# Performance work log

Hardware: AMD Instinct MI355X
Metric: run time of the kernel (lower is better)

The kernel has to match this reference:

```python
import jax, jax.numpy as jnp
import numpy as np
from jax import lax

WINDOW_SIZE = 11
SIGMA = 1.5
LEVELS = 5
WEIGHTS = jnp.array([0.0448, 0.2856, 0.3001, 0.2363, 0.1333], dtype=jnp.float32)


def _make_window(ws, channel):
    # 1D gaussian, sigma=1.5, normalized; outer product -> 2D window, tiled per channel
    x = jnp.arange(ws, dtype=jnp.float32) - ws // 2
    g = jnp.exp(-(x * x) / (2.0 * SIGMA * SIGMA))
    g = g / g.sum()
    w2 = jnp.outer(g, g)  # [ws, ws]
    return jnp.broadcast_to(w2[None, None], (channel, 1, ws, ws))


def _dwconv(x, win, channel):
    # depthwise VALID conv, matches F.conv2d(..., padding=0, groups=channel)
    return lax.conv_general_dilated(
        x, win, window_strides=(1, 1), padding='VALID',
        feature_group_count=channel,
        dimension_numbers=('NCHW', 'OIHW', 'NCHW'))


def _ssim_cs(img1, img2):
    # dynamic data range, as in the torch source (L=1 for [0,1) inputs)
    max_val = jnp.where(jnp.max(img1) > 128.0, 255.0, 1.0)
    min_val = jnp.where(jnp.min(img1) < -0.5, -1.0, 0.0)
    L = max_val - min_val

    n, c, h, w = img1.shape
    ws = min(WINDOW_SIZE, h, w)  # static python int
    win = _make_window(ws, c)

    mu1 = _dwconv(img1, win, c)
    mu2 = _dwconv(img2, win, c)
    mu1_sq = mu1 * mu1
    mu2_sq = mu2 * mu2
    mu1_mu2 = mu1 * mu2
    sigma1_sq = _dwconv(img1 * img1, win, c) - mu1_sq
    sigma2_sq = _dwconv(img2 * img2, win, c) - mu2_sq
    sigma12 = _dwconv(img1 * img2, win, c) - mu1_mu2

    C1 = (0.01 * L) ** 2
    C2 = (0.03 * L) ** 2
    v1 = 2.0 * sigma12 + C2
    v2 = sigma1_sq + sigma2_sq + C2
    cs = jnp.mean(v1 / v2)
    ssim_map = (2.0 * mu1_mu2 + C1) * v1 / ((mu1_sq + mu2_sq + C1) * v2)
    return jnp.mean(ssim_map), cs


def _avg_pool2(x):
    # F.avg_pool2d(x, (2,2)): stride 2, no padding (floors odd dims)
    n, c, h, w = x.shape
    x = x[:, :, : (h // 2) * 2, : (w // 2) * 2]
    return x.reshape(n, c, h // 2, 2, w // 2, 2).mean(axis=(3, 5))


def setup_inputs() -> dict:
    key = jax.random.key(0)
    k1, k2 = jax.random.split(key)
    img1 = jax.random.uniform(k1, (16, 3, 512, 512), dtype=jnp.float32)
    img2 = jax.random.uniform(k2, (16, 3, 512, 512), dtype=jnp.float32)
    return {"img1": img1, "img2": img2}


def reference(img1, img2):
    mssim, mcs = [], []
    for _ in range(LEVELS):  # fixed 5-level pyramid, shapes shrink each level
        s, c = _ssim_cs(img1, img2)
        mssim.append(s)
        mcs.append(c)
        img1 = _avg_pool2(img1)
        img2 = _avg_pool2(img2)
    mssim = (jnp.stack(mssim) + 1.0) / 2.0  # normalize=True
    mcs = (jnp.stack(mcs) + 1.0) / 2.0
    pow1 = mcs ** WEIGHTS
    pow2 = mssim ** WEIGHTS
    # NOTE: faithful to source: prod over (pow1[:-1] * pow2[-1]) broadcasts pow2[-1]
    return jnp.prod(pow1[:-1] * pow2[-1])
```

## Files before the change

### kernel.cpp

```cpp
#include <hip/hip_runtime.h>


#define NTHR 512

typedef float v4  __attribute__((ext_vector_type(4)));
typedef float v2f __attribute__((ext_vector_type(2)));

__device__ __forceinline__ float frcp(float x) { return __builtin_amdgcn_rcpf(x); }

#define GW_DEF const float GW[11] = {0.00102840f, 0.00759877f, 0.03600070f, \
    0.10936069f, 0.21300636f, 0.26601172f, 0.21300636f, 0.10936069f,        \
    0.03600070f, 0.00759877f, 0.00102840f};

__device__ __forceinline__ void conv11(const float* s, const float* d,
                                       v4& hs, v4& hd, v4& hss, v4& hdd)
{
    GW_DEF
    #pragma unroll
    for (int j = 0; j < 11; ++j) {
        float w = GW[j];
        v4 sv = {s[j], s[j+1], s[j+2], s[j+3]};
        v4 dv = {d[j], d[j+1], d[j+2], d[j+3]};
        v4 wsv = w * sv, wdv = w * dv;
        hs += wsv; hd += wdv; hss += wsv * sv; hdd += wdv * dv;
    }
}

template<int TROWS>
__device__ void hpass_direct(const float* __restrict__ p1, const float* __restrict__ p2,
                             int H, int tx0, int ty0, v4* hb)
{
    constexpr int HR = TROWS + 10;
    for (int task = threadIdx.x; task < HR * 8; task += NTHR) {
        const int r = task >> 3, cg2 = task & 7;
        const int gr = ty0 + r;
        const int c0 = tx0 + cg2 * 4;
        v4 hs = 0.f, hd = 0.f, hss = 0.f, hdd = 0.f;
        if (gr < H) {
            float s[16], d[16];
            if (c0 + 16 <= H) {
                const float* pa = p1 + (size_t)gr * H + c0;
                const float* pb = p2 + (size_t)gr * H + c0;
                #pragma unroll
                for (int q = 0; q < 4; ++q) {
                    v4 va = *(const v4*)(pa + 4 * q);
                    v4 vb = *(const v4*)(pb + 4 * q);
                    v4 sv = va + vb, dv = va - vb;
                    s[4*q+0] = sv.x; s[4*q+1] = sv.y; s[4*q+2] = sv.z; s[4*q+3] = sv.w;
                    d[4*q+0] = dv.x; d[4*q+1] = dv.y; d[4*q+2] = dv.z; d[4*q+3] = dv.w;
                }
            } else {
                #pragma unroll
                for (int q = 0; q < 16; ++q) {
                    int cc = c0 + q;
                    float a = (cc < H) ? p1[(size_t)gr * H + cc] : 0.f;
                    float b = (cc < H) ? p2[(size_t)gr * H + cc] : 0.f;
                    s[q] = a + b; d[q] = a - b;
                }
            }
            conv11(s, d, hs, hd, hss, hdd);
        }
        v4* row = &hb[r * 33 + cg2 * 4];
        row[0] = (v4){hs.x, hd.x, hss.x, hdd.x};
        row[1] = (v4){hs.y, hd.y, hss.y, hdd.y};
        row[2] = (v4){hs.z, hd.z, hss.z, hdd.z};
        row[3] = (v4){hs.w, hd.w, hss.w, hdd.w};
    }
}

template<int TROWS>
__device__ void hpass_pool1(const float* __restrict__ q1, const float* __restrict__ q2,
                            int H, int tx0, int ty0, v4* hb)
{
    constexpr int HR = TROWS + 10;
    const int HS = 2 * H;
    for (int task = threadIdx.x; task < HR * 8; task += NTHR) {
        const int r = task >> 3, cg2 = task & 7;
        const int gr = ty0 + r;
        const int c0 = tx0 + cg2 * 4;
        v4 hs = 0.f, hd = 0.f, hss = 0.f, hdd = 0.f;
        if (gr < H) {
            float s[16], d[16];
            const int iy = 2 * gr;
            if (c0 + 16 <= H) {
                const float* a0 = q1 + (size_t)iy * HS + 2 * c0;
                const float* b0 = q2 + (size_t)iy * HS + 2 * c0;
                #pragma unroll
                for (int q = 0; q < 8; ++q) {
                    v4 xa0 = *(const v4*)(a0 + 4 * q);
                    v4 xa1 = *(const v4*)(a0 + HS + 4 * q);
                    v4 xb0 = *(const v4*)(b0 + 4 * q);
                    v4 xb1 = *(const v4*)(b0 + HS + 4 * q);
                    float pa0 = 0.25f * ((xa0.x + xa0.y) + (xa1.x + xa1.y));
                    float pa1 = 0.25f * ((xa0.z + xa0.w) + (xa1.z + xa1.w));
                    float pb0 = 0.25f * ((xb0.x + xb0.y) + (xb1.x + xb1.y));
                    float pb1 = 0.25f * ((xb0.z + xb0.w) + (xb1.z + xb1.w));
                    s[2*q]   = pa0 + pb0; d[2*q]   = pa0 - pb0;
                    s[2*q+1] = pa1 + pb1; d[2*q+1] = pa1 - pb1;
                }
            } else {
                #pragma unroll
                for (int q = 0; q < 16; ++q) {
                    int cc = c0 + q;
                    float pa = 0.f, pb = 0.f;
                    if (cc < H) {
                        const float* qa = q1 + (size_t)iy * HS + 2 * cc;
                        const float* qb = q2 + (size_t)iy * HS + 2 * cc;
                        pa = 0.25f * ((qa[0] + qa[1]) + (qa[HS] + qa[HS + 1]));
                        pb = 0.25f * ((qb[0] + qb[1]) + (qb[HS] + qb[HS + 1]));
                    }
                    s[q] = pa + pb; d[q] = pa - pb;
                }
            }
            conv11(s, d, hs, hd, hss, hdd);
        }
        v4* row = &hb[r * 33 + cg2 * 4];
        row[0] = (v4){hs.x, hd.x, hss.x, hdd.x};
        row[1] = (v4){hs.y, hd.y, hss.y, hdd.y};
        row[2] = (v4){hs.z, hd.z, hss.z, hdd.z};
        row[3] = (v4){hs.w, hd.w, hss.w, hdd.w};
    }
}

template<int TROWS>
__device__ void hpass_lds(const float* la, const float* lb,
                          int H, int tx0, int ty0, v4* hb)
{
    constexpr int HR = TROWS + 10;
    for (int task = threadIdx.x; task < HR * 8; task += NTHR) {
        const int r = task >> 3, cg2 = task & 7;
        const int gr = ty0 + r;
        const int c0 = tx0 + cg2 * 4;
        v4 hs = 0.f, hd = 0.f, hss = 0.f, hdd = 0.f;
        if (gr < H) {
            float s[16], d[16];
            const int lr = 2 * r;
            #pragma unroll
            for (int q = 0; q < 16; ++q) {
                int cc = c0 + q;
                float pa = 0.f, pb = 0.f;
                if (cc < H) {
                    int lc = 2 * (cc - tx0);
                    const float* a0 = la + lr * 89 + lc;
                    const float* b0 = lb + lr * 89 + lc;
                    pa = 0.25f * ((a0[0] + a0[1]) + (a0[89] + a0[90]));
                    pb = 0.25f * ((b0[0] + b0[1]) + (b0[89] + b0[90]));
                }
                s[q] = pa + pb; d[q] = pa - pb;
            }
            conv11(s, d, hs, hd, hss, hdd);
        }
        v4* row = &hb[r * 33 + cg2 * 4];
        row[0] = (v4){hs.x, hd.x, hss.x, hdd.x};
        row[1] = (v4){hs.y, hd.y, hss.y, hdd.y};
        row[2] = (v4){hs.z, hd.z, hss.z, hdd.z};
        row[3] = (v4){hs.w, hd.w, hss.w, hdd.w};
    }
}

__device__ void stage_pool1(const float* __restrict__ s1, const float* __restrict__ s2,
                            int DL, int tx0, int ty0, float* la, float* lb)
{
    const int SD = 2 * DL;
    for (int t = threadIdx.x; t < 2 * 52 * 44; t += NTHR) {
        int im = t >= 52 * 44; int tt = im ? t - 52 * 44 : t;
        int rr = tt / 44, cp = tt % 44;
        int xr = 2 * ty0 + rr, xc = 2 * tx0 + 2 * cp;
        const float* sp = im ? s2 : s1;
        float* lp = im ? lb : la;
        float v0 = 0.f, v1 = 0.f;
        if (xr < DL && xc < DL) {
            const float* q0 = sp + (size_t)(2 * xr) * SD + 2 * xc;
            v4 r0 = *(const v4*)q0;
            v4 r1 = *(const v4*)(q0 + SD);
            v0 = 0.25f * ((r0.x + r0.y) + (r1.x + r1.y));
            v1 = 0.25f * ((r0.z + r0.w) + (r1.z + r1.w));
        }
        lp[rr * 89 + 2 * cp]     = v0;
        lp[rr * 89 + 2 * cp + 1] = v1;
    }
}

__device__ void stage_pool2(const float* __restrict__ s1, const float* __restrict__ s2,
                            int DL, int ty0, float* la, float* lb)
{
    const int SD = 4 * DL;
    for (int t = threadIdx.x; t < 2 * 52 * 88; t += NTHR) {
        int im = t >= 52 * 88; int tt = im ? t - 52 * 88 : t;
        int rr = tt / 88, cc = tt % 88;
        int yr = 2 * ty0 + rr, yc = cc;
        const float* sp = im ? s2 : s1;
        float* lp = im ? lb : la;
        float v = 0.f;
        if (yr < DL && yc < DL) {
            const float* q = sp + (size_t)(4 * yr) * SD + 4 * yc;
            v4 r0 = *(const v4*)q;
            v4 r1 = *(const v4*)(q + SD);
            v4 r2 = *(const v4*)(q + 2 * SD);
            v4 r3 = *(const v4*)(q + 3 * SD);
            float a00 = 0.25f * ((r0.x + r0.y) + (r1.x + r1.y));
            float a01 = 0.25f * ((r0.z + r0.w) + (r1.z + r1.w));
            float a10 = 0.25f * ((r2.x + r2.y) + (r3.x + r3.y));
            float a11 = 0.25f * ((r2.z + r2.w) + (r3.z + r3.w));
            v = 0.25f * ((a00 + a01) + (a10 + a11));
        }
        lp[rr * 89 + cc] = v;
    }
}

template<int TROWS>
__device__ void vpass_reduce(int H, int tx0, int ty0, const v4* hb, float* red,
                             float* __restrict__ partS, float* __restrict__ partC)
{
    constexpr int OPT = TROWS * 32 / NTHR;
    constexpr int NW  = NTHR / 64;
    GW_DEF
    const float C1 = 1e-4f, C2 = 9e-4f;
    const int tid   = threadIdx.x;
    const int outHW = H - 10;
    const int col   = tid & 31;
    const int row0  = (tid >> 5) * OPT;
    const float colm = (tx0 + col < outHW) ? 1.f : 0.f;
    v4 A[OPT];
    #pragma unroll
    for (int k = 0; k < OPT; ++k) A[k] = 0.f;

    #pragma unroll
    for (int r = 0; r < OPT + 10; ++r) {
        v4 h = hb[(row0 + r) * 33 + col];
        #pragma unroll
        for (int k = 0; k < OPT; ++k) {
            const int j = r - k;
            if (j >= 0 && j < 11) A[k] += GW[j] * h;
        }
    }

    float ssim_t = 0.f, cs_t = 0.f;
    #pragma unroll
    for (int k = 0; k < OPT; ++k) {
        float mask = colm * ((ty0 + row0 + k < outHW) ? 1.f : 0.f);
        float mu_s = A[k].x, mu_d = A[k].y;
        float P = mu_s * mu_s, Q = mu_d * mu_d;
        float U = A[k].z - P, V = A[k].w - Q;
        float v1 = 0.5f * (U - V) + C2;
        float v2 = 0.5f * (U + V) + C2;
        float n1 = 0.5f * (P - Q) + C1;
        float d1 = 0.5f * (P + Q) + C1;
        float csv = v1 * frcp(v2);
        float ssv = n1 * csv * frcp(d1);
        cs_t   += mask * csv;
        ssim_t += mask * ssv;
    }

    #pragma unroll
    for (int off = 32; off > 0; off >>= 1) {
        ssim_t += __shfl_down(ssim_t, off);
        cs_t   += __shfl_down(cs_t, off);
    }
    int wave = tid >> 6, lane = tid & 63;
    if (lane == 0) { red[wave] = ssim_t; red[NW + wave] = cs_t; }
    __syncthreads();
    if (tid == 0) {
        float s = 0.f, c = 0.f;
        #pragma unroll
        for (int w = 0; w < NW; ++w) { s += red[w]; c += red[NW + w]; }
        partS[0] = s; partC[0] = c;
    }
}

__global__ __launch_bounds__(NTHR, 8) void l0_kernel(
    const float* __restrict__ img1, const float* __restrict__ img2,
    float* __restrict__ x1a, float* __restrict__ x1b,
    float* __restrict__ accS, float* __restrict__ accC)
{
    __shared__ v4 hb[74 * 33];
    __shared__ float red[16];

    const int tid = threadIdx.x;
    const int nc  = blockIdx.z;
    const int tx0 = blockIdx.x * 32;
    const int ty0 = blockIdx.y * 64;
    const int H   = 512;
    const float* p1 = img1 + (size_t)nc * H * H;
    const float* p2 = img2 + (size_t)nc * H * H;

    {
        const int r = tid >> 4, c = tid & 15;
        const int iy = ty0 + 2 * r, ix = tx0 + 2 * c;
        v2f a0 = *(const v2f*)(p1 + (size_t)iy * H + ix);
        v2f a1 = *(const v2f*)(p1 + (size_t)(iy + 1) * H + ix);
        v2f b0 = *(const v2f*)(p2 + (size_t)iy * H + ix);
        v2f b1 = *(const v2f*)(p2 + (size_t)(iy + 1) * H + ix);
        size_t o = (size_t)nc * 256 * 256 + (size_t)((ty0 >> 1) + r) * 256 + ((tx0 >> 1) + c);
        x1a[o] = 0.25f * ((a0.x + a0.y) + (a1.x + a1.y));
        x1b[o] = 0.25f * ((b0.x + b0.y) + (b1.x + b1.y));
    }

    hpass_direct<64>(p1, p2, H, tx0, ty0, hb);
    __syncthreads();
    int fb = (int)blockIdx.x + 16 * ((int)blockIdx.y + 8 * nc);
    vpass_reduce<64>(H, tx0, ty0, hb, red, accS + fb, accC + fb);
}

__global__ __launch_bounds__(NTHR, 6) void tail_kernel(
    const float* __restrict__ x1a, const float* __restrict__ x1b,
    float* __restrict__ accTS, float* __restrict__ accTC)
{
    __shared__ v4 smemv[3172];
    __shared__ float red[16];
    v4* hb    = smemv;
    float* la = (float*)smemv + 3432;
    float* lb = la + 52 * 89;

    const int b = (int)blockIdx.x;
    if (b < 1536) {
        const int H = 256;
        int cx = b & 7, rem = b >> 3, cy = rem & 3, nc = rem >> 2;
        const float* p1 = x1a + (size_t)nc * H * H;
        const float* p2 = x1b + (size_t)nc * H * H;
        int tx0 = cx * 32, ty0 = cy * 64;
        hpass_direct<64>(p1, p2, H, tx0, ty0, hb);
        __syncthreads();
        vpass_reduce<64>(H, tx0, ty0, hb, red, accTS + b, accTC + b);
    } else if (b < 2304) {
        const int H = 128;
        int lbk = b - 1536;
        int cx = lbk & 3, rem = lbk >> 2, cy = rem & 3, nc = rem >> 2;
        const float* q1 = x1a + (size_t)nc * 256 * 256;
        const float* q2 = x1b + (size_t)nc * 256 * 256;
        int tx0 = cx * 32, ty0 = cy * 32;
        hpass_pool1<32>(q1, q2, H, tx0, ty0, hb);
        __syncthreads();
        vpass_reduce<32>(H, tx0, ty0, hb, red, accTS + b, accTC + b);
    } else if (b < 2688) {
        const int H = 64;
        int lbk = b - 2304;
        int cx = lbk & 1, rem = lbk >> 1, cy = rem & 3, nc = rem >> 2;
        const float* q1 = x1a + (size_t)nc * 256 * 256;
        const float* q2 = x1b + (size_t)nc * 256 * 256;
        int tx0 = cx * 32, ty0 = cy * 16;
        stage_pool1(q1, q2, 128, tx0, ty0, la, lb);
        __syncthreads();
        hpass_lds<16>(la, lb, H, tx0, ty0, hb);
        __syncthreads();
        vpass_reduce<16>(H, tx0, ty0, hb, red, accTS + b, accTC + b);
    } else {
        const int H = 32;
        int lbk = b - 2688;
        int cy = lbk & 1, nc = lbk >> 1;
        const float* q1 = x1a + (size_t)nc * 256 * 256;
        const float* q2 = x1b + (size_t)nc * 256 * 256;
        int tx0 = 0, ty0 = cy * 16;
        stage_pool2(q1, q2, 64, ty0, la, lb);
        __syncthreads();
        hpass_lds<16>(la, lb, H, tx0, ty0, hb);
        __syncthreads();
        vpass_reduce<16>(H, tx0, ty0, hb, red, accTS + b, accTC + b);
    }
}

__global__ void finalize_kernel(const float* __restrict__ acc0S, const float* __restrict__ acc0C,
                                const float* __restrict__ accTS, const float* __restrict__ accTC,
                                float* __restrict__ out)
{
    __shared__ float sm[10];
    __shared__ float wred[8];
    const int tid  = (int)threadIdx.x;
    const int wave = tid >> 6, lane = tid & 63;
    const int st[5] = {0, 0, 1536, 2304, 2688};
    const int en[5] = {6144, 1536, 2304, 2688, 2784};

    for (int srs = 0; srs < 10; ++srs) {
        int l = srs >> 1;
        const float* base = (srs & 1) ? (l == 0 ? acc0C : accTC)
                                      : (l == 0 ? acc0S : accTS);
        float p = 0.f;
        for (int i = st[l] + tid; i < en[l]; i += NTHR) p += base[i];
        #pragma unroll
        for (int o = 32; o > 0; o >>= 1) p += __shfl_down(p, o);
        if (lane == 0) wred[wave] = p;
        __syncthreads();
        if (tid == 0) {
            float t = 0.f;
            #pragma unroll
            for (int w = 0; w < 8; ++w) t += wred[w];
            sm[srs] = t;
        }
        __syncthreads();
    }

    if (tid == 0) {
        const float w[5] = {0.0448f, 0.2856f, 0.3001f, 0.2363f, 0.1333f};
        float ms[5], mc[5];
        for (int l = 0; l < 5; ++l) {
            int oh = (512 >> l) - 10;
            float cnt = 48.f * (float)oh * (float)oh;
            ms[l] = (sm[2 * l] / cnt + 1.f) * 0.5f;
            mc[l] = (sm[2 * l + 1] / cnt + 1.f) * 0.5f;
        }
        float p2 = powf(ms[4], w[4]);
        float r = 1.f;
        for (int i = 0; i < 4; ++i) r *= powf(mc[i], w[i]) * p2;
        out[0] = r;
    }
}

extern "C" void kernel_launch(void* const* d_in, const int* in_sizes, int n_in,
                              void* d_out, int out_size, void* d_ws, size_t ws_size,
                              hipStream_t stream)
{
    (void)in_sizes; (void)n_in; (void)out_size; (void)ws_size;
    const float* img1 = (const float*)d_in[0];
    const float* img2 = (const float*)d_in[1];
    float* out = (float*)d_out;
    float* ws  = (float*)d_ws;

    float* acc0S = ws;
    float* acc0C = acc0S + 6144;
    float* accTS = acc0C + 6144;
    float* accTC = accTS + 2784;
    float* x1a   = accTC + 2784;
    float* x1b   = x1a + (size_t)48 * 256 * 256;

    l0_kernel<<<dim3(16, 8, 48), NTHR, 0, stream>>>(img1, img2, x1a, x1b, acc0S, acc0C);
    tail_kernel<<<dim3(2784), NTHR, 0, stream>>>(x1a, x1b, accTS, accTC);
    finalize_kernel<<<1, NTHR, 0, stream>>>(acc0S, acc0C, accTS, accTC, out);
}
```

Before: 225.9 us.

## Fuse all pyramid levels into one kernel reading original images directly

Merges the level-0 kernel and the tail kernel into a single launch in which every pyramid level recomputes its pooled input straight from the full-resolution images, so the intermediate 256x256 pooled buffers are no longer written or read. Block indices are ordered with the smallest, deepest levels first and the full-resolution blocks last, and a new 8x8 pooling stage is added for the coarsest level. This drops one kernel launch, the dependency between the two kernels, and the round trip of the intermediate buffers. In exchange, deeper levels read more raw data per output (up to 64 pixels per pooled value) with strided access, and the level-0 blocks now run with a lower occupancy bound.

```diff
diff --git a/kernel.cpp b/kernel.cpp
--- a/kernel.cpp
+++ b/kernel.cpp
@@ -159,9 +159,8 @@
 }
 
 __device__ void stage_pool1(const float* __restrict__ s1, const float* __restrict__ s2,
-                            int DL, int tx0, int ty0, float* la, float* lb)
-{
-    const int SD = 2 * DL;
+                            int SD, int DB, int tx0, int ty0, float* la, float* lb)
+{
     for (int t = threadIdx.x; t < 2 * 52 * 44; t += NTHR) {
         int im = t >= 52 * 44; int tt = im ? t - 52 * 44 : t;
         int rr = tt / 44, cp = tt % 44;
@@ -169,7 +168,7 @@
         const float* sp = im ? s2 : s1;
         float* lp = im ? lb : la;
         float v0 = 0.f, v1 = 0.f;
-        if (xr < DL && xc < DL) {
+        if (xr < DB && xc < DB) {
             const float* q0 = sp + (size_t)(2 * xr) * SD + 2 * xc;
             v4 r0 = *(const v4*)q0;
             v4 r1 = *(const v4*)(q0 + SD);
@@ -182,17 +181,16 @@
 }
 
 __device__ void stage_pool2(const float* __restrict__ s1, const float* __restrict__ s2,
-                            int DL, int ty0, float* la, float* lb)
-{
-    const int SD = 4 * DL;
+                            int SD, int DB, int tx0, int ty0, float* la, float* lb)
+{
     for (int t = threadIdx.x; t < 2 * 52 * 88; t += NTHR) {
         int im = t >= 52 * 88; int tt = im ? t - 52 * 88 : t;
         int rr = tt / 88, cc = tt % 88;
-        int yr = 2 * ty0 + rr, yc = cc;
+        int yr = 2 * ty0 + rr, yc = 2 * tx0 + cc;
         const float* sp = im ? s2 : s1;
         float* lp = im ? lb : la;
         float v = 0.f;
-        if (yr < DL && yc < DL) {
+        if (yr < DB && yc < DB) {
             const float* q = sp + (size_t)(4 * yr) * SD + 4 * yc;
             v4 r0 = *(const v4*)q;
             v4 r1 = *(const v4*)(q + SD);
@@ -203,6 +201,47 @@
             float a10 = 0.25f * ((r2.x + r2.y) + (r3.x + r3.y));
             float a11 = 0.25f * ((r2.z + r2.w) + (r3.z + r3.w));
             v = 0.25f * ((a00 + a01) + (a10 + a11));
+        }
+        lp[rr * 89 + cc] = v;
+    }
+}
+
+__device__ void stage_pool3(const float* __restrict__ s1, const float* __restrict__ s2,
+                            int SD, int DB, int tx0, int ty0, float* la, float* lb)
+{
+    for (int t = threadIdx.x; t < 2 * 52 * 88; t += NTHR) {
+        int im = t >= 52 * 88; int tt = im ? t - 52 * 88 : t;
+        int rr = tt / 88, cc = tt % 88;
+        int yr = 2 * ty0 + rr, yc = 2 * tx0 + cc;
+        const float* sp = im ? s2 : s1;
+        float* lp = im ? lb : la;
+        float v = 0.f;
+        if (yr < DB && yc < DB) {
+            const float* q = sp + (size_t)(8 * yr) * SD + 8 * yc;
+            float p2h[2][2];
+            #pragma unroll
+            for (int h = 0; h < 2; ++h) {
+                const float* qq = q + (size_t)(4 * h) * SD;
+                v4 A0 = *(const v4*)qq;
+                v4 A1 = *(const v4*)(qq + SD);
+                v4 A2 = *(const v4*)(qq + 2 * SD);
+                v4 A3 = *(const v4*)(qq + 3 * SD);
+                v4 B0 = *(const v4*)(qq + 4);
+                v4 B1 = *(const v4*)(qq + SD + 4);
+                v4 B2 = *(const v4*)(qq + 2 * SD + 4);
+                v4 B3 = *(const v4*)(qq + 3 * SD + 4);
+                float p00 = 0.25f * ((A0.x + A0.y) + (A1.x + A1.y));
+                float p01 = 0.25f * ((A0.z + A0.w) + (A1.z + A1.w));
+                float p10 = 0.25f * ((A2.x + A2.y) + (A3.x + A3.y));
+                float p11 = 0.25f * ((A2.z + A2.w) + (A3.z + A3.w));
+                float q00 = 0.25f * ((B0.x + B0.y) + (B1.x + B1.y));
+                float q01 = 0.25f * ((B0.z + B0.w) + (B1.z + B1.w));
+                float q10 = 0.25f * ((B2.x + B2.y) + (B3.x + B3.y));
+                float q11 = 0.25f * ((B2.z + B2.w) + (B3.z + B3.w));
+                p2h[h][0] = 0.25f * ((p00 + p01) + (p10 + p11));
+                p2h[h][1] = 0.25f * ((q00 + q01) + (q10 + q11));
+            }
+            v = 0.25f * ((p2h[0][0] + p2h[0][1]) + (p2h[1][0] + p2h[1][1]));
         }
         lp[rr * 89 + cc] = v;
     }
@@ -268,43 +307,9 @@
     }
 }
 
-__global__ __launch_bounds__(NTHR, 8) void l0_kernel(
+__global__ __launch_bounds__(NTHR, 6) void conv_kernel(
     const float* __restrict__ img1, const float* __restrict__ img2,
-    float* __restrict__ x1a, float* __restrict__ x1b,
     float* __restrict__ accS, float* __restrict__ accC)
-{
-    __shared__ v4 hb[74 * 33];
-    __shared__ float red[16];
-
-    const int tid = threadIdx.x;
-    const int nc  = blockIdx.z;
-    const int tx0 = blockIdx.x * 32;
-    const int ty0 = blockIdx.y * 64;
-    const int H   = 512;
-    const float* p1 = img1 + (size_t)nc * H * H;
-    const float* p2 = img2 + (size_t)nc * H * H;
-
-    {
-        const int r = tid >> 4, c = tid & 15;
-        const int iy = ty0 + 2 * r, ix = tx0 + 2 * c;
-        v2f a0 = *(const v2f*)(p1 + (size_t)iy * H + ix);
-        v2f a1 = *(const v2f*)(p1 + (size_t)(iy + 1) * H + ix);
-        v2f b0 = *(const v2f*)(p2 + (size_t)iy * H + ix);
-        v2f b1 = *(const v2f*)(p2 + (size_t)(iy + 1) * H + ix);
-        size_t o = (size_t)nc * 256 * 256 + (size_t)((ty0 >> 1) + r) * 256 + ((tx0 >> 1) + c);
-        x1a[o] = 0.25f * ((a0.x + a0.y) + (a1.x + a1.y));
-        x1b[o] = 0.25f * ((b0.x + b0.y) + (b1.x + b1.y));
-    }
-
-    hpass_direct<64>(p1, p2, H, tx0, ty0, hb);
-    __syncthreads();
-    int fb = (int)blockIdx.x + 16 * ((int)blockIdx.y + 8 * nc);
-    vpass_reduce<64>(H, tx0, ty0, hb, red, accS + fb, accC + fb);
-}
-
-__global__ __launch_bounds__(NTHR, 6) void tail_kernel(
-    const float* __restrict__ x1a, const float* __restrict__ x1b,
-    float* __restrict__ accTS, float* __restrict__ accTC)
 {
     __shared__ v4 smemv[3172];
     __shared__ float red[16];
@@ -313,67 +318,74 @@
     float* lb = la + 52 * 89;
 
     const int b = (int)blockIdx.x;
-    if (b < 1536) {
-        const int H = 256;
-        int cx = b & 7, rem = b >> 3, cy = rem & 3, nc = rem >> 2;
-        const float* p1 = x1a + (size_t)nc * H * H;
-        const float* p2 = x1b + (size_t)nc * H * H;
+    const size_t IMS = (size_t)512 * 512;
+
+    if (b >= 3552) {
+        int lbk = b - 3552;
+        int cx = lbk & 15, rem = lbk >> 4, cy = rem & 7, nc = rem >> 3;
+        const float* p1 = img1 + (size_t)nc * IMS;
+        const float* p2 = img2 + (size_t)nc * IMS;
         int tx0 = cx * 32, ty0 = cy * 64;
-        hpass_direct<64>(p1, p2, H, tx0, ty0, hb);
-        __syncthreads();
-        vpass_reduce<64>(H, tx0, ty0, hb, red, accTS + b, accTC + b);
-    } else if (b < 2304) {
-        const int H = 128;
-        int lbk = b - 1536;
-        int cx = lbk & 3, rem = lbk >> 2, cy = rem & 3, nc = rem >> 2;
-        const float* q1 = x1a + (size_t)nc * 256 * 256;
-        const float* q2 = x1b + (size_t)nc * 256 * 256;
-        int tx0 = cx * 32, ty0 = cy * 32;
-        hpass_pool1<32>(q1, q2, H, tx0, ty0, hb);
-        __syncthreads();
-        vpass_reduce<32>(H, tx0, ty0, hb, red, accTS + b, accTC + b);
-    } else if (b < 2688) {
-        const int H = 64;
-        int lbk = b - 2304;
+        hpass_direct<64>(p1, p2, 512, tx0, ty0, hb);
+        __syncthreads();
+        vpass_reduce<64>(512, tx0, ty0, hb, red, accS + b, accC + b);
+    } else if (b >= 2016) {
+        int lbk = b - 2016;
+        int cx = lbk & 7, rem = lbk >> 3, cy = rem & 3, nc = rem >> 2;
+        const float* p1 = img1 + (size_t)nc * IMS;
+        const float* p2 = img2 + (size_t)nc * IMS;
+        int tx0 = cx * 32, ty0 = cy * 64;
+        hpass_pool1<64>(p1, p2, 256, tx0, ty0, hb);
+        __syncthreads();
+        vpass_reduce<64>(256, tx0, ty0, hb, red, accS + b, accC + b);
+    } else if (b >= 480) {
+        int lbk = b - 480;
+        int cx = lbk & 3, rem = lbk >> 2, cy = rem & 7, nc = rem >> 3;
+        const float* p1 = img1 + (size_t)nc * IMS;
+        const float* p2 = img2 + (size_t)nc * IMS;
+        int tx0 = cx * 32, ty0 = cy * 16;
+        stage_pool1(p1, p2, 512, 256, tx0, ty0, la, lb);
+        __syncthreads();
+        hpass_lds<16>(la, lb, 128, tx0, ty0, hb);
+        __syncthreads();
+        vpass_reduce<16>(128, tx0, ty0, hb, red, accS + b, accC + b);
+    } else if (b >= 96) {
+        int lbk = b - 96;
         int cx = lbk & 1, rem = lbk >> 1, cy = rem & 3, nc = rem >> 2;
-        const float* q1 = x1a + (size_t)nc * 256 * 256;
-        const float* q2 = x1b + (size_t)nc * 256 * 256;
+        const float* p1 = img1 + (size_t)nc * IMS;
+        const float* p2 = img2 + (size_t)nc * IMS;
         int tx0 = cx * 32, ty0 = cy * 16;
-        stage_pool1(q1, q2, 128, tx0, ty0, la, lb);
-        __syncthreads();
-        hpass_lds<16>(la, lb, H, tx0, ty0, hb);
-        __syncthreads();
-        vpass_reduce<16>(H, tx0, ty0, hb, red, accTS + b, accTC + b);
+        stage_pool2(p1, p2, 512, 128, tx0, ty0, la, lb);
+        __syncthreads();
+        hpass_lds<16>(la, lb, 64, tx0, ty0, hb);
+        __syncthreads();
+        vpass_reduce<16>(64, tx0, ty0, hb, red, accS + b, accC + b);
     } else {
-        const int H = 32;
-        int lbk = b - 2688;
-        int cy = lbk & 1, nc = lbk >> 1;
-        const float* q1 = x1a + (size_t)nc * 256 * 256;
-        const float* q2 = x1b + (size_t)nc * 256 * 256;
+        int cy = b & 1, nc = b >> 1;
+        const float* p1 = img1 + (size_t)nc * IMS;
+        const float* p2 = img2 + (size_t)nc * IMS;
         int tx0 = 0, ty0 = cy * 16;
-        stage_pool2(q1, q2, 64, ty0, la, lb);
-        __syncthreads();
-        hpass_lds<16>(la, lb, H, tx0, ty0, hb);
-        __syncthreads();
-        vpass_reduce<16>(H, tx0, ty0, hb, red, accTS + b, accTC + b);
-    }
-}
-
-__global__ void finalize_kernel(const float* __restrict__ acc0S, const float* __restrict__ acc0C,
-                                const float* __restrict__ accTS, const float* __restrict__ accTC,
+        stage_pool3(p1, p2, 512, 64, tx0, ty0, la, lb);
+        __syncthreads();
+        hpass_lds<16>(la, lb, 32, tx0, ty0, hb);
+        __syncthreads();
+        vpass_reduce<16>(32, tx0, ty0, hb, red, accS + b, accC + b);
+    }
+}
+
+__global__ void finalize_kernel(const float* __restrict__ accS, const float* __restrict__ accC,
                                 float* __restrict__ out)
 {
     __shared__ float sm[10];
     __shared__ float wred[8];
     const int tid  = (int)threadIdx.x;
     const int wave = tid >> 6, lane = tid & 63;
-    const int st[5] = {0, 0, 1536, 2304, 2688};
-    const int en[5] = {6144, 1536, 2304, 2688, 2784};
+    const int st[5] = {3552, 2016, 480, 96, 0};
+    const int en[5] = {9696, 3552, 2016, 480, 96};
 
     for (int srs = 0; srs < 10; ++srs) {
         int l = srs >> 1;
-        const float* base = (srs & 1) ? (l == 0 ? acc0C : accTC)
-                                      : (l == 0 ? acc0S : accTS);
+        const float* base = (srs & 1) ? accC : accS;
         float p = 0.f;
         for (int i = st[l] + tid; i < en[l]; i += NTHR) p += base[i];
         #pragma unroll
@@ -415,14 +427,9 @@
     float* out = (float*)d_out;
     float* ws  = (float*)d_ws;
 
-    float* acc0S = ws;
-    float* acc0C = acc0S + 6144;
-    float* accTS = acc0C + 6144;
-    float* accTC = accTS + 2784;
-    float* x1a   = accTC + 2784;
-    float* x1b   = x1a + (size_t)48 * 256 * 256;
-
-    l0_kernel<<<dim3(16, 8, 48), NTHR, 0, stream>>>(img1, img2, x1a, x1b, acc0S, acc0C);
-    tail_kernel<<<dim3(2784), NTHR, 0, stream>>>(x1a, x1b, accTS, accTC);
-    finalize_kernel<<<1, NTHR, 0, stream>>>(acc0S, acc0C, accTS, accTC, out);
-}
+    float* accS = ws;
+    float* accC = accS + 9696;
+
+    conv_kernel<<<dim3(9696), NTHR, 0, stream>>>(img1, img2, accS, accC);
+    finalize_kernel<<<1, NTHR, 0, stream>>>(accS, accC, out);
+}
```

After: 289.6 us. 28.2% more time.
